# Kernel optimization log

Measured on AMD Instinct MI355X. Metric: run time of the kernel, lower is better.

The kernel has to match this reference:

```python
import jax, jax.numpy as jnp
import numpy as np

EPS = 1e-5

def binarize(w):
    # sign() binarization with straight-through estimator (identity grad)
    s = jnp.where(w >= 0, 1.0, -1.0).astype(w.dtype)
    return w + jax.lax.stop_gradient(s - w)

def batchnorm(x, gamma, beta):
    # BatchNorm1d in training mode: biased batch statistics over axis 0
    mean = jnp.mean(x, axis=0)
    var = jnp.mean(jnp.square(x - mean), axis=0)
    return (x - mean) * jax.lax.rsqrt(var + EPS) * gamma + beta

def setup_inputs() -> dict:
    key = jax.random.key(0)
    ks = jax.random.split(key, 3)
    B, D_IN, D_H, D_OUT = 65536, 784, 300, 10
    x = jax.random.normal(ks[0], (B, D_IN), dtype=jnp.float32)
    W1 = jax.random.normal(ks[1], (D_H, D_IN), dtype=jnp.float32) * 0.05
    W2 = jax.random.normal(ks[2], (D_OUT, D_H), dtype=jnp.float32) * 0.05
    gamma1 = jnp.ones((D_H,), jnp.float32)
    beta1 = jnp.zeros((D_H,), jnp.float32)
    gamma2 = jnp.ones((D_OUT,), jnp.float32)
    beta2 = jnp.zeros((D_OUT,), jnp.float32)
    return {"x": x, "W1": W1, "gamma1": gamma1, "beta1": beta1,
            "W2": W2, "gamma2": gamma2, "beta2": beta2}

def reference(x, W1, gamma1, beta1, W2, gamma2, beta2):
    h = x @ binarize(W1).T            # [B, 300]
    h = batchnorm(h, gamma1, beta1)
    o = h @ binarize(W2).T            # [B, 10]
    return batchnorm(o, gamma2, beta2)
```

## Files before the change

kernel.cpp:

```cpp
#include <hip/hip_runtime.h>
#include <cstdint>
#include <cstddef>

#define B_ROWS 65536
#define D_IN   784
#define KP     800
#define D_H    300
#define NP     320
#define D_OUT  10
#define NP2    16
#define EPS    1e-5f
#define NBLK   1024
#define APAD   44

typedef _Float16 half8  __attribute__((ext_vector_type(8)));
typedef float    floatx4 __attribute__((ext_vector_type(4)));

#define OFF_S1   ((size_t)0)
#define OFF_H    ((size_t)512000)
#define OFF_ST1  (OFF_H + (size_t)41943040)
#define OFF_W2   (OFF_ST1 + (size_t)2560)
#define OFF_ST2  (OFF_W2 + (size_t)10240)
#define OFF_OC   (OFF_ST2 + (size_t)256)
#define OFF_P1   OFF_OC
#define OFF_P2   (OFF_OC + (size_t)4194304)

__global__ void k_prep1(const float* __restrict__ W1, _Float16* __restrict__ S1)
{
    int idx = blockIdx.x * 256 + threadIdx.x;
    int n = idx / KP;
    int k = idx - n * KP;
    float v = 0.0f;
    if (n < D_H && k < D_IN)
        v = (W1[n * D_IN + k] >= 0.0f) ? 1.0f : -1.0f;
    S1[idx] = (_Float16)v;
}


#define PF_B(BV, NK)                                                        \
    _Pragma("unroll")                                                       \
    for (int nt = 0; nt < 5; ++nt)                                          \
        BV[nt] = *(const half8*)(bb + (size_t)nt * 16 * KP + (NK));

#define STAGE_LOAD(V0, V1, KK)                                              \
    {                                                                       \
        V0 = (floatx4){}; V1 = (floatx4){};                                 \
        if ((KK) + sc < D_IN) {               \
            V0 = *(const floatx4*)(sxp + (KK));                             \
            V1 = *(const floatx4*)(sxp + (KK) + 4);                         \
        }                                                                   \
    }

#define STAGE_STORE(V0, V1, BUF)                                            \
    {                                                                       \
        half8 hv;                                                           \
        _Pragma("unroll")                                                   \
        for (int i2 = 0; i2 < 4; ++i2) {                                    \
            hv[i2]     = (_Float16)V0[i2];                                  \
            hv[4 + i2] = (_Float16)V1[i2];                                  \
        }                                                                   \
        *(half8*)&Alds[BUF][srow][sc] = hv;                                 \
    }

#define AFRAG(BUF)                                                          \
    _Pragma("unroll")                                                       \
    for (int mt = 0; mt < 4; ++mt)                                          \
        a[mt] = *(const half8*)&Alds[BUF][mt * 16 + row15][quad * 8];

#define COMPUTE(BV)                                                         \
    _Pragma("unroll")                                                       \
    for (int nt = 0; nt < 5; ++nt)                                          \
        _Pragma("unroll")                                                   \
        for (int mt = 0; mt < 4; ++mt)                                      \
            acc[mt][nt] = __builtin_amdgcn_mfma_f32_16x16x32_f16(           \
                a[mt], BV[nt], acc[mt][nt], 0, 0, 0);

#define BAR()                                                               \
    asm volatile("s_waitcnt lgkmcnt(0)" ::: "memory");                      \
    __builtin_amdgcn_sched_barrier(0);                                      \
    __builtin_amdgcn_s_barrier();                                           \
    __builtin_amdgcn_sched_barrier(0);

__global__ __launch_bounds__(256) void k_gemm1(const float* __restrict__ x,
                                               const _Float16* __restrict__ S1,
                                               _Float16* __restrict__ h,
                                               float* __restrict__ part)
{
    __shared__ _Float16 Alds[2][64][APAD];
    const int t     = threadIdx.x;
    const int wave  = t >> 6;
    const int lane  = t & 63;
    const int row15 = lane & 15;
    const int quad  = lane >> 4;
    const int m0    = blockIdx.x * 64;

    const int srow = t >> 2;
    const int sc   = (t & 3) * 8;
    const float* sxp = x + (size_t)(m0 + srow) * D_IN + sc;

    const _Float16* bb = S1 + (size_t)(wave * 80 + row15) * KP + quad * 8;

    floatx4 acc[4][5] = {};
    half8   b0[5], b1[5];
    half8   a[4];
    floatx4 a0, a1, c0, c1;

    STAGE_LOAD(a0, a1, 0)
    PF_B(b0, 0)
    STAGE_LOAD(c0, c1, 32)
    STAGE_STORE(a0, a1, 0)
    BAR()

    for (int i = 0; i < 12; ++i) {
        const int kk = i * 64;
        STAGE_LOAD(a0, a1, kk + 64)
        PF_B(b1, kk + 32)
        AFRAG(0)
        COMPUTE(b0)
        STAGE_STORE(c0, c1, 1)
        BAR()
        STAGE_LOAD(c0, c1, kk + 96)
        PF_B(b0, kk + 64)
        AFRAG(1)
        COMPUTE(b1)
        STAGE_STORE(a0, a1, 0)
        BAR()
    }
    AFRAG(0)
    COMPUTE(b0)

    float s[5] = {}, q[5] = {};
#pragma unroll
    for (int mt = 0; mt < 4; ++mt)
#pragma unroll
        for (int nt = 0; nt < 5; ++nt)
#pragma unroll
            for (int r = 0; r < 4; ++r) {
                float v = acc[mt][nt][r];
                int m = m0 + mt * 16 + quad * 4 + r;
                int n = wave * 80 + nt * 16 + row15;
                h[(size_t)m * NP + n] = (_Float16)v;
                s[nt] += v;
                q[nt] += v * v;
            }
#pragma unroll
    for (int nt = 0; nt < 5; ++nt) {
        s[nt] += __shfl_xor(s[nt], 16); s[nt] += __shfl_xor(s[nt], 32);
        q[nt] += __shfl_xor(q[nt], 16); q[nt] += __shfl_xor(q[nt], 32);
    }
    if (quad == 0) {
#pragma unroll
        for (int nt = 0; nt < 5; ++nt) {
            int col = wave * 80 + nt * 16 + row15;
            part[(size_t)col * NBLK + blockIdx.x]        = s[nt];
            part[(size_t)(NP + col) * NBLK + blockIdx.x] = q[nt];
        }
    }
}

__global__ void k_reduce(const float* __restrict__ part, float* __restrict__ st)
{
    __shared__ float red[4];
    const int c = blockIdx.x;
    const int t = threadIdx.x;
    const float* p = part + (size_t)c * NBLK;
    float s = p[t] + p[t + 256] + p[t + 512] + p[t + 768];
#pragma unroll
    for (int off = 1; off < 64; off <<= 1) s += __shfl_xor(s, off);
    if ((t & 63) == 0) red[t >> 6] = s;
    __syncthreads();
    if (t == 0) st[c] = red[0] + red[1] + red[2] + red[3];
}

__global__ void k_prep2(const float* __restrict__ st, const float* __restrict__ gamma1,
                        const float* __restrict__ W2, _Float16* __restrict__ w2h)
{
    int j = threadIdx.x;
    float mean = st[j] * (1.0f / 65536.0f);
    float var  = st[NP + j] * (1.0f / 65536.0f) - mean * mean;
    float a1   = 0.0f;
    if (j < D_H) a1 = gamma1[j] / sqrtf(var + EPS);
    for (int k = 0; k < NP2; ++k) {
        float w = 0.0f;
        if (k < D_OUT && j < D_H)
            w = (W2[k * D_H + j] >= 0.0f) ? a1 : -a1;
        w2h[k * NP + j] = (_Float16)w;
    }
}

__global__ __launch_bounds__(256) void k_gemm2(const _Float16* __restrict__ h,
                                               const _Float16* __restrict__ w2h,
                                               float* __restrict__ oc,
                                               float* __restrict__ part2)
{
    __shared__ _Float16 Wlds[16][328];
    __shared__ float reds[4][16], redq[4][16];
    const int t     = threadIdx.x;
    const int wave  = t >> 6;
    const int lane  = t & 63;
    const int row15 = lane & 15;
    const int quad  = lane >> 4;

    for (int c = t; c < 640; c += 256) {
        int r  = c / 40;
        int cc = (c - r * 40) * 8;
        *(half8*)&Wlds[r][cc] = *(const half8*)(w2h + r * NP + cc);
    }
    __syncthreads();

    const int m0 = blockIdx.x * 64 + wave * 16;
    const _Float16* hp = h + (size_t)(m0 + row15) * NP + quad * 8;
    floatx4 acc = {};
#pragma unroll
    for (int kk = 0; kk < NP; kk += 32) {
        half8 a2 = *(const half8*)(hp + kk);
        half8 b2 = *(const half8*)&Wlds[row15][kk + quad * 8];
        acc = __builtin_amdgcn_mfma_f32_16x16x32_f16(a2, b2, acc, 0, 0, 0);
    }
    float s = 0.f, q = 0.f;
#pragma unroll
    for (int r = 0; r < 4; ++r) {
        float v = acc[r];
        oc[(size_t)(m0 + quad * 4 + r) * NP2 + row15] = v;
        s += v; q += v * v;
    }
    s += __shfl_xor(s, 16); s += __shfl_xor(s, 32);
    q += __shfl_xor(q, 16); q += __shfl_xor(q, 32);
    if (lane < 16) { reds[wave][row15] = s; redq[wave][row15] = q; }
    __syncthreads();
    if (t < 16) {
        float S = reds[0][t] + reds[1][t] + reds[2][t] + reds[3][t];
        float Q = redq[0][t] + redq[1][t] + redq[2][t] + redq[3][t];
        part2[(size_t)t * NBLK + blockIdx.x]          = S;
        part2[(size_t)(16 + t) * NBLK + blockIdx.x]   = Q;
    }
}

__global__ void k_final(const float* __restrict__ oc, const float* __restrict__ st2,
                        const float* __restrict__ gamma2, const float* __restrict__ beta2,
                        float* __restrict__ out)
{
    int idx = blockIdx.x * 256 + threadIdx.x;
    int m = idx / 10;
    int k = idx - m * 10;
    float mean = st2[k] * (1.0f / 65536.0f);
    float var  = st2[16 + k] * (1.0f / 65536.0f) - mean * mean;
    float sc   = gamma2[k] / sqrtf(var + EPS);
    out[idx] = (oc[(size_t)m * NP2 + k] - mean) * sc + beta2[k];
}

extern "C" void kernel_launch(void* const* d_in, const int* in_sizes, int n_in,
                              void* d_out, int out_size, void* d_ws, size_t ws_size,
                              hipStream_t stream)
{
    const float* x      = (const float*)d_in[0];
    const float* W1     = (const float*)d_in[1];
    const float* gamma1 = (const float*)d_in[2];
    const float* W2     = (const float*)d_in[4];
    const float* gamma2 = (const float*)d_in[5];
    const float* beta2  = (const float*)d_in[6];
    float* out = (float*)d_out;

    char* ws = (char*)d_ws;
    _Float16* S1    = (_Float16*)(ws + OFF_S1);
    _Float16* h     = (_Float16*)(ws + OFF_H);
    float*    st1   = (float*)(ws + OFF_ST1);
    _Float16* w2h   = (_Float16*)(ws + OFF_W2);
    float*    st2   = (float*)(ws + OFF_ST2);
    float*    oc    = (float*)(ws + OFF_OC);
    float*    part  = (float*)(ws + OFF_P1);
    float*    part2 = (float*)(ws + OFF_P2);

    k_prep1 <<<1000, 256, 0, stream>>>(W1, S1);
    k_gemm1 <<<NBLK, 256, 0, stream>>>(x, S1, h, part);
    k_reduce<<<640, 256, 0, stream>>>(part, st1);
    k_prep2 <<<1, 320, 0, stream>>>(st1, gamma1, W2, w2h);
    k_gemm2 <<<NBLK, 256, 0, stream>>>(h, w2h, oc, part2);
    k_reduce<<<32, 256, 0, stream>>>(part2, st2);
    k_final <<<2560, 256, 0, stream>>>(oc, st2, gamma2, beta2, out);
}
```

Measured before the change: 111.2 us.

## Double the GEMM1 K-stage to 64 with two LDS subtiles per buffer

```diff
diff --git a/kernel.cpp b/kernel.cpp
--- a/kernel.cpp
+++ b/kernel.cpp
@@ -4,7 +4,7 @@
 
 #define B_ROWS 65536
 #define D_IN   784
-#define KP     800
+#define KP     832
 #define D_H    300
 #define NP     320
 #define D_OUT  10
@@ -17,13 +17,13 @@
 typedef float    floatx4 __attribute__((ext_vector_type(4)));
 
 #define OFF_S1   ((size_t)0)
-#define OFF_H    ((size_t)512000)
+#define OFF_H    ((size_t)532480)
 #define OFF_ST1  (OFF_H + (size_t)41943040)
 #define OFF_W2   (OFF_ST1 + (size_t)2560)
 #define OFF_ST2  (OFF_W2 + (size_t)10240)
 #define OFF_OC   (OFF_ST2 + (size_t)256)
 #define OFF_P1   OFF_OC
-#define OFF_P2   (OFF_OC + (size_t)4194304)
+#define OFF_P2   OFF_S1
 
 __global__ void k_prep1(const float* __restrict__ W1, _Float16* __restrict__ S1)
 {
@@ -37,35 +37,40 @@
 }
 
 
-#define PF_B(BV, NK)                                                        \
+#define PFB(NK)                                                             \
     _Pragma("unroll")                                                       \
     for (int nt = 0; nt < 5; ++nt)                                          \
-        BV[nt] = *(const half8*)(bb + (size_t)nt * 16 * KP + (NK));
-
-#define STAGE_LOAD(V0, V1, KK)                                              \
+        bS0[nt] = *(const half8*)(bb + (size_t)nt * 16 * KP + (NK));        \
+    _Pragma("unroll")                                                       \
+    for (int nt = 0; nt < 5; ++nt)                                          \
+        bS1[nt] = *(const half8*)(bb + (size_t)nt * 16 * KP + (NK) + 32);
+
+#define LOADA(SET, KK)                                                      \
+    _Pragma("unroll")                                                       \
+    for (int j = 0; j < 4; ++j) {                                           \
+        SET[j] = (floatx4){};                                               \
+        if ((KK) + sc < D_IN)                                               \
+            SET[j] = *(const floatx4*)(sxp + (KK) + 4 * j);                 \
+    }
+
+#define STOREA(SET, P)                                                      \
     {                                                                       \
-        V0 = (floatx4){}; V1 = (floatx4){};                                 \
-        if ((KK) + sc < D_IN) {               \
-            V0 = *(const floatx4*)(sxp + (KK));                             \
-            V1 = *(const floatx4*)(sxp + (KK) + 4);                         \
+        half8 h0, h1;                                                       \
+        _Pragma("unroll")                                                   \
+        for (int j = 0; j < 4; ++j) {                                       \
+            h0[j]     = (_Float16)SET[0][j];                                \
+            h0[4 + j] = (_Float16)SET[1][j];                                \
+            h1[j]     = (_Float16)SET[2][j];                                \
+            h1[4 + j] = (_Float16)SET[3][j];                                \
         }                                                                   \
-    }
-
-#define STAGE_STORE(V0, V1, BUF)                                            \
-    {                                                                       \
-        half8 hv;                                                           \
-        _Pragma("unroll")                                                   \
-        for (int i2 = 0; i2 < 4; ++i2) {                                    \
-            hv[i2]     = (_Float16)V0[i2];                                  \
-            hv[4 + i2] = (_Float16)V1[i2];                                  \
-        }                                                                   \
-        *(half8*)&Alds[BUF][srow][sc] = hv;                                 \
-    }
-
-#define AFRAG(BUF)                                                          \
+        *(half8*)&Alds[(P) + stile][srow][scol]     = h0;                   \
+        *(half8*)&Alds[(P) + stile][srow][scol + 8] = h1;                   \
+    }
+
+#define AFRAG(P, KS)                                                        \
     _Pragma("unroll")                                                       \
     for (int mt = 0; mt < 4; ++mt)                                          \
-        a[mt] = *(const half8*)&Alds[BUF][mt * 16 + row15][quad * 8];
+        a[mt] = *(const half8*)&Alds[(P) + (KS)][mt * 16 + row15][quad * 8];
 
 #define COMPUTE(BV)                                                         \
     _Pragma("unroll")                                                       \
@@ -86,7 +91,7 @@
                                                _Float16* __restrict__ h,
                                                float* __restrict__ part)
 {
-    __shared__ _Float16 Alds[2][64][APAD];
+    __shared__ _Float16 Alds[4][64][APAD];
     const int t     = threadIdx.x;
     const int wave  = t >> 6;
     const int lane  = t & 63;
@@ -94,40 +99,49 @@
     const int quad  = lane >> 4;
     const int m0    = blockIdx.x * 64;
 
-    const int srow = t >> 2;
-    const int sc   = (t & 3) * 8;
+    const int srow  = t >> 2;
+    const int q4    = t & 3;
+    const int sc    = q4 * 16;
+    const int stile = q4 >> 1;
+    const int scol  = (q4 & 1) * 16;
     const float* sxp = x + (size_t)(m0 + srow) * D_IN + sc;
 
     const _Float16* bb = S1 + (size_t)(wave * 80 + row15) * KP + quad * 8;
 
     floatx4 acc[4][5] = {};
-    half8   b0[5], b1[5];
+    half8   bS0[5], bS1[5];
     half8   a[4];
-    floatx4 a0, a1, c0, c1;
-
-    STAGE_LOAD(a0, a1, 0)
-    PF_B(b0, 0)
-    STAGE_LOAD(c0, c1, 32)
-    STAGE_STORE(a0, a1, 0)
+    floatx4 sA[4], sB[4];
+
+    LOADA(sA, 0)
+    LOADA(sB, 64)
+    STOREA(sA, 0)
     BAR()
 
-    for (int i = 0; i < 12; ++i) {
-        const int kk = i * 64;
-        STAGE_LOAD(a0, a1, kk + 64)
-        PF_B(b1, kk + 32)
-        AFRAG(0)
-        COMPUTE(b0)
-        STAGE_STORE(c0, c1, 1)
+    for (int i = 0; i < 6; ++i) {
+        const int kk = i * 128;
+        PFB(kk)
+        LOADA(sA, kk + 128)
+        AFRAG(0, 0)
+        COMPUTE(bS0)
+        AFRAG(0, 1)
+        COMPUTE(bS1)
+        STOREA(sB, 2)
         BAR()
-        STAGE_LOAD(c0, c1, kk + 96)
-        PF_B(b0, kk + 64)
-        AFRAG(1)
-        COMPUTE(b1)
-        STAGE_STORE(a0, a1, 0)
+        PFB(kk + 64)
+        LOADA(sB, kk + 192)
+        AFRAG(2, 0)
+        COMPUTE(bS0)
+        AFRAG(2, 1)
+        COMPUTE(bS1)
+        STOREA(sA, 0)
         BAR()
     }
-    AFRAG(0)
-    COMPUTE(b0)
+    PFB(768)
+    AFRAG(0, 0)
+    COMPUTE(bS0)
+    AFRAG(0, 1)
+    COMPUTE(bS1)
 
     float s[5] = {}, q[5] = {};
 #pragma unroll
@@ -271,7 +285,7 @@
     float*    part  = (float*)(ws + OFF_P1);
     float*    part2 = (float*)(ws + OFF_P2);
 
-    k_prep1 <<<1000, 256, 0, stream>>>(W1, S1);
+    k_prep1 <<<1040, 256, 0, stream>>>(W1, S1);
     k_gemm1 <<<NBLK, 256, 0, stream>>>(x, S1, h, part);
     k_reduce<<<640, 256, 0, stream>>>(part, st1);
     k_prep2 <<<1, 320, 0, stream>>>(st1, gamma1, W2, w2h);
```

New measurement: 125.0 us. +12.4%, slower.

## Split gemm1 block into 8 waves with 2x4 M/N wave tiling

Applied to the files above, without the earlier changes.

```diff
diff --git a/kernel.cpp b/kernel.cpp
--- a/kernel.cpp
+++ b/kernel.cpp
@@ -14,6 +14,7 @@
 #define APAD   44
 
 typedef _Float16 half8  __attribute__((ext_vector_type(8)));
+typedef _Float16 half4  __attribute__((ext_vector_type(4)));
 typedef float    floatx4 __attribute__((ext_vector_type(4)));
 
 #define OFF_S1   ((size_t)0)
@@ -42,36 +43,31 @@
     for (int nt = 0; nt < 5; ++nt)                                          \
         BV[nt] = *(const half8*)(bb + (size_t)nt * 16 * KP + (NK));
 
-#define STAGE_LOAD(V0, V1, KK)                                              \
+#define STAGE_LOAD(V, KK)                                                   \
     {                                                                       \
-        V0 = (floatx4){}; V1 = (floatx4){};                                 \
-        if ((KK) + sc < D_IN) {               \
-            V0 = *(const floatx4*)(sxp + (KK));                             \
-            V1 = *(const floatx4*)(sxp + (KK) + 4);                         \
-        }                                                                   \
-    }
-
-#define STAGE_STORE(V0, V1, BUF)                                            \
+        V = (floatx4){};                                                    \
+        if ((KK) + scol < D_IN)                                             \
+            V = *(const floatx4*)(sxp + (KK));                              \
+    }
+
+#define STAGE_STORE(V, BUF)                                                 \
     {                                                                       \
-        half8 hv;                                                           \
+        half4 hv;                                                           \
         _Pragma("unroll")                                                   \
-        for (int i2 = 0; i2 < 4; ++i2) {                                    \
-            hv[i2]     = (_Float16)V0[i2];                                  \
-            hv[4 + i2] = (_Float16)V1[i2];                                  \
-        }                                                                   \
-        *(half8*)&Alds[BUF][srow][sc] = hv;                                 \
+        for (int j = 0; j < 4; ++j) hv[j] = (_Float16)V[j];                 \
+        *(half4*)&Alds[BUF][srow][scol] = hv;                               \
     }
 
 #define AFRAG(BUF)                                                          \
     _Pragma("unroll")                                                       \
-    for (int mt = 0; mt < 4; ++mt)                                          \
-        a[mt] = *(const half8*)&Alds[BUF][mt * 16 + row15][quad * 8];
+    for (int mt = 0; mt < 2; ++mt)                                          \
+        a[mt] = *(const half8*)&Alds[BUF][wm * 32 + mt * 16 + row15][quad * 8];
 
 #define COMPUTE(BV)                                                         \
     _Pragma("unroll")                                                       \
     for (int nt = 0; nt < 5; ++nt)                                          \
         _Pragma("unroll")                                                   \
-        for (int mt = 0; mt < 4; ++mt)                                      \
+        for (int mt = 0; mt < 2; ++mt)                                      \
             acc[mt][nt] = __builtin_amdgcn_mfma_f32_16x16x32_f16(           \
                 a[mt], BV[nt], acc[mt][nt], 0, 0, 0);
 
@@ -81,10 +77,10 @@
     __builtin_amdgcn_s_barrier();                                           \
     __builtin_amdgcn_sched_barrier(0);
 
-__global__ __launch_bounds__(256) void k_gemm1(const float* __restrict__ x,
-                                               const _Float16* __restrict__ S1,
-                                               _Float16* __restrict__ h,
-                                               float* __restrict__ part)
+__global__ __launch_bounds__(512, 3) void k_gemm1(const float* __restrict__ x,
+                                                  const _Float16* __restrict__ S1,
+                                                  _Float16* __restrict__ h,
+                                                  float* __restrict__ part)
 {
     __shared__ _Float16 Alds[2][64][APAD];
     const int t     = threadIdx.x;
@@ -92,38 +88,40 @@
     const int lane  = t & 63;
     const int row15 = lane & 15;
     const int quad  = lane >> 4;
+    const int wm    = wave >> 2;
+    const int wn    = wave & 3;
     const int m0    = blockIdx.x * 64;
 
-    const int srow = t >> 2;
-    const int sc   = (t & 3) * 8;
-    const float* sxp = x + (size_t)(m0 + srow) * D_IN + sc;
-
-    const _Float16* bb = S1 + (size_t)(wave * 80 + row15) * KP + quad * 8;
-
-    floatx4 acc[4][5] = {};
+    const int srow  = t >> 3;
+    const int scol  = (t & 7) * 4;
+    const float* sxp = x + (size_t)(m0 + srow) * D_IN + scol;
+
+    const _Float16* bb = S1 + (size_t)(wn * 80 + row15) * KP + quad * 8;
+
+    floatx4 acc[2][5] = {};
     half8   b0[5], b1[5];
-    half8   a[4];
-    floatx4 a0, a1, c0, c1;
-
-    STAGE_LOAD(a0, a1, 0)
+    half8   a[2];
+    floatx4 svA, svB;
+
+    STAGE_LOAD(svA, 0)
     PF_B(b0, 0)
-    STAGE_LOAD(c0, c1, 32)
-    STAGE_STORE(a0, a1, 0)
+    STAGE_LOAD(svB, 32)
+    STAGE_STORE(svA, 0)
     BAR()
 
     for (int i = 0; i < 12; ++i) {
         const int kk = i * 64;
-        STAGE_LOAD(a0, a1, kk + 64)
+        STAGE_LOAD(svA, kk + 64)
         PF_B(b1, kk + 32)
         AFRAG(0)
         COMPUTE(b0)
-        STAGE_STORE(c0, c1, 1)
+        STAGE_STORE(svB, 1)
         BAR()
-        STAGE_LOAD(c0, c1, kk + 96)
+        STAGE_LOAD(svB, kk + 96)
         PF_B(b0, kk + 64)
         AFRAG(1)
         COMPUTE(b1)
-        STAGE_STORE(a0, a1, 0)
+        STAGE_STORE(svA, 0)
         BAR()
     }
     AFRAG(0)
@@ -131,14 +129,14 @@
 
     float s[5] = {}, q[5] = {};
 #pragma unroll
-    for (int mt = 0; mt < 4; ++mt)
+    for (int mt = 0; mt < 2; ++mt)
 #pragma unroll
         for (int nt = 0; nt < 5; ++nt)
 #pragma unroll
             for (int r = 0; r < 4; ++r) {
                 float v = acc[mt][nt][r];
-                int m = m0 + mt * 16 + quad * 4 + r;
-                int n = wave * 80 + nt * 16 + row15;
+                int m = m0 + wm * 32 + mt * 16 + quad * 4 + r;
+                int n = wn * 80 + nt * 16 + row15;
                 h[(size_t)m * NP + n] = (_Float16)v;
                 s[nt] += v;
                 q[nt] += v * v;
@@ -148,12 +146,23 @@
         s[nt] += __shfl_xor(s[nt], 16); s[nt] += __shfl_xor(s[nt], 32);
         q[nt] += __shfl_xor(q[nt], 16); q[nt] += __shfl_xor(q[nt], 32);
     }
-    if (quad == 0) {
+    float* red = (float*)&Alds[0][0][0];
+    __syncthreads();
+    if (wm == 1 && quad == 0) {
 #pragma unroll
         for (int nt = 0; nt < 5; ++nt) {
-            int col = wave * 80 + nt * 16 + row15;
-            part[(size_t)col * NBLK + blockIdx.x]        = s[nt];
-            part[(size_t)(NP + col) * NBLK + blockIdx.x] = q[nt];
+            int cl = wn * 80 + nt * 16 + row15;
+            red[cl]       = s[nt];
+            red[320 + cl] = q[nt];
+        }
+    }
+    __syncthreads();
+    if (wm == 0 && quad == 0) {
+#pragma unroll
+        for (int nt = 0; nt < 5; ++nt) {
+            int cl = wn * 80 + nt * 16 + row15;
+            part[(size_t)cl * NBLK + blockIdx.x]        = s[nt] + red[cl];
+            part[(size_t)(NP + cl) * NBLK + blockIdx.x] = q[nt] + red[320 + cl];
         }
     }
 }
@@ -272,7 +281,7 @@
     float*    part2 = (float*)(ws + OFF_P2);
 
     k_prep1 <<<1000, 256, 0, stream>>>(W1, S1);
-    k_gemm1 <<<NBLK, 256, 0, stream>>>(x, S1, h, part);
+    k_gemm1 <<<NBLK, 512, 0, stream>>>(x, S1, h, part);
     k_reduce<<<640, 256, 0, stream>>>(part, st1);
     k_prep2 <<<1, 320, 0, stream>>>(st1, gamma1, W2, w2h);
     k_gemm2 <<<NBLK, 256, 0, stream>>>(h, w2h, oc, part2);
```

Result: slower. 140.5 us (+26.4%).
